# Kernel tuning notes

Hardware: AMD Instinct MI355X
Metric: run time of the kernel (lower is better)

The kernel has to match this reference:

```python
import jax, jax.numpy as jnp
import numpy as np

B, T, D = 2, 4096, 768
H = 12
HD = D // H  # 64
SCALE = 1.0 / np.sqrt(HD)


def setup_inputs() -> dict:
    key = jax.random.key(0)
    k1, k2, k3 = jax.random.split(key, 3)
    x = jax.random.normal(k1, (B, T, D), dtype=jnp.float32)
    W_qkv = jax.random.normal(k2, (D, 3 * D), dtype=jnp.float32) * (1.0 / np.sqrt(D))
    b_qkv = jnp.zeros((3 * D,), dtype=jnp.float32)
    W_out = jax.random.normal(k3, (D, D), dtype=jnp.float32) * (1.0 / np.sqrt(D))
    b_out = jnp.zeros((D,), dtype=jnp.float32)
    return {"x": x, "W_qkv": W_qkv, "b_qkv": b_qkv, "W_out": W_out, "b_out": b_out}


def reference(x, W_qkv, b_qkv, W_out, b_out):
    Bx, Tx, C = x.shape
    qkv = x @ W_qkv + b_qkv                                  # [B,T,3D]
    qkv = qkv.reshape(Bx, Tx, 3, H, HD).transpose(2, 0, 3, 1, 4)  # [3,B,H,T,hd]
    q, k, v = qkv[0], qkv[1], qkv[2]
    scores = jnp.einsum('bhqd,bhkd->bhqk', q, k) * SCALE      # [B,H,T,T]
    causal = jnp.tril(jnp.ones((Tx, Tx), dtype=bool))
    scores = jnp.where(causal[None, None], scores, -jnp.inf)
    attn = jax.nn.softmax(scores, axis=-1)
    out = jnp.einsum('bhqk,bhkd->bhqd', attn, v)              # [B,H,T,hd]
    out = out.transpose(0, 2, 1, 3).reshape(Bx, Tx, C)        # [B,T,D]
    return out @ W_out + b_out
```

## Files before the change

### kernel.cpp

```cpp
#include <hip/hip_runtime.h>
#include <cstdint>
#include <cstddef>

typedef _Float16 f16x8 __attribute__((ext_vector_type(8)));
typedef _Float16 f16x4 __attribute__((ext_vector_type(4)));
typedef float    f32x4 __attribute__((ext_vector_type(4)));

#define AS_GLOBAL __attribute__((address_space(1)))
#define AS_LDS    __attribute__((address_space(3)))

__device__ __forceinline__ void load16_to_lds(const _Float16* g, _Float16* l) {
    __builtin_amdgcn_global_load_lds((const AS_GLOBAL void*)g, (AS_LDS void*)l, 16, 0, 0);
}

#define BB   2
#define TT   4096
#define DD   768
#define NH   12
#define HDIM 64
#define D3   2304
#define SC2  (0.125f * 1.44269504088896f)

__global__ __launch_bounds__(256) void prep(const float* __restrict__ x,
                                            _Float16* __restrict__ Xh,
                                            const float* __restrict__ Wqkv,
                                            _Float16* __restrict__ Wqkvt,
                                            const float* __restrict__ Wout,
                                            _Float16* __restrict__ Wot) {
    const int bid = blockIdx.x, tid = threadIdx.x;
    if (bid < 6144) {
        const int i = bid * 1024 + tid * 4;
        float4 v = *(const float4*)(x + i);
        f16x4 h;
        h[0] = (_Float16)v.x; h[1] = (_Float16)v.y;
        h[2] = (_Float16)v.z; h[3] = (_Float16)v.w;
        *(f16x4*)(Xh + i) = h;
        return;
    }
    __shared__ float tile[32][33];
    const float* in; _Float16* out; int C, bx, by;
    if (bid < 7872) {
        const int t = bid - 6144;
        in = Wqkv; out = Wqkvt; C = 2304;
        bx = (t % 72) * 32; by = (t / 72) * 32;
    } else {
        const int t = bid - 7872;
        in = Wout; out = Wot; C = 768;
        bx = (t % 24) * 32; by = (t / 24) * 32;
    }
    const int R = 768;
    const int tx = tid & 31, ty = tid >> 5;
#pragma unroll
    for (int j = 0; j < 32; j += 8)
        tile[ty + j][tx] = in[(size_t)(by + ty + j) * C + bx + tx];
    __syncthreads();
#pragma unroll
    for (int j = 0; j < 32; j += 8)
        out[(size_t)(bx + ty + j) * R + by + tx] = (_Float16)tile[tx][ty + j];
}

template <typename OutT>
__device__ __forceinline__ void gemm_body(const _Float16* __restrict__ A,
                                          const _Float16* __restrict__ Bt,
                                          const float* __restrict__ bias, bool bias_row,
                                          OutT* __restrict__ C, int N, int K,
                                          int m0, int n0,
                                          _Float16* As, _Float16* Bs) {
    const int tid  = threadIdx.x;
    const int wave = tid >> 6, lane = tid & 63, quad = lane >> 4, l16 = lane & 15;
    const int wm = (wave & 1) * 64, wn = (wave >> 1) * 64;
    const int rowc = lane >> 3, part = lane & 7;

    f32x4 acc[4][4];
#pragma unroll
    for (int i = 0; i < 4; ++i)
#pragma unroll
        for (int n = 0; n < 4; ++n) acc[i][n] = f32x4{0.f, 0.f, 0.f, 0.f};

    for (int k0 = 0; k0 < K; k0 += 64) {
        __syncthreads();
#pragma unroll
        for (int cc = 0; cc < 4; ++cc) {
            const int ch = wave * 4 + cc;
            load16_to_lds(A  + (size_t)(m0 + ch * 8 + rowc) * K + k0 + part * 8,
                          As + ch * 512);
            load16_to_lds(Bt + (size_t)(n0 + ch * 8 + rowc) * K + k0 + part * 8,
                          Bs + ch * 512);
        }
        __syncthreads();
#pragma unroll
        for (int i = 0; i < 4; ++i) {
            f16x8 a0 = *(const f16x8*)(As + (wm + i * 16 + l16) * 64 + quad * 8);
            f16x8 a1 = *(const f16x8*)(As + (wm + i * 16 + l16) * 64 + 32 + quad * 8);
#pragma unroll
            for (int n = 0; n < 4; ++n) {
                f16x8 b0 = *(const f16x8*)(Bs + (wn + n * 16 + l16) * 64 + quad * 8);
                f16x8 b1 = *(const f16x8*)(Bs + (wn + n * 16 + l16) * 64 + 32 + quad * 8);
                acc[i][n] = __builtin_amdgcn_mfma_f32_16x16x32_f16(a0, b0, acc[i][n], 0, 0, 0);
                acc[i][n] = __builtin_amdgcn_mfma_f32_16x16x32_f16(a1, b1, acc[i][n], 0, 0, 0);
            }
        }
    }
#pragma unroll
    for (int i = 0; i < 4; ++i)
#pragma unroll
        for (int n = 0; n < 4; ++n)
#pragma unroll
            for (int r = 0; r < 4; ++r) {
                const int row = m0 + wm + i * 16 + quad * 4 + r;
                const int col = n0 + wn + n * 16 + l16;
                const float bv = bias_row ? bias[row] : bias[col];
                C[(size_t)row * N + col] = (OutT)(acc[i][n][r] + bv);
            }
}

__global__ __launch_bounds__(256) void gemm_qkv(const _Float16* __restrict__ Xh,
                                                const _Float16* __restrict__ Wqkvt,
                                                const float* __restrict__ bqkv,
                                                _Float16* __restrict__ QKh,
                                                _Float16* __restrict__ VtG) {
    __shared__ __align__(16) _Float16 As[128 * 64];
    __shared__ __align__(16) _Float16 Bs[128 * 64];
    const int bid = blockIdx.x;
    if (bid < 768) {
        const int xcd = bid & 7, j = bid >> 3;
        const int by = xcd + 8 * (j / 12);
        const int bx = j % 12;
        gemm_body<_Float16>(Xh, Wqkvt, bqkv, false, QKh, 1536, DD,
                            by * 128, bx * 128, As, Bs);
    } else {
        const int t = bid - 768;
        const int xcd = t & 7, j = t >> 3;
        const int bx = xcd + 8 * (j / 6);
        const int by = j % 6;
        gemm_body<_Float16>(Wqkvt + (size_t)1536 * DD, Xh, bqkv + 1536, true, VtG,
                            8192, DD, by * 128, bx * 128, As, Bs);
    }
}

__global__ __launch_bounds__(256) void gemm_out(const _Float16* __restrict__ A,
                                                const _Float16* __restrict__ Bt,
                                                const float* __restrict__ bias,
                                                float* __restrict__ C) {
    __shared__ __align__(16) _Float16 As[64 * 64];
    __shared__ __align__(16) _Float16 Bs[128 * 64];
    const int L = blockIdx.x;
    const int xcd = L & 7, j = L >> 3;
    const int by = xcd + 8 * (j / 6);
    const int bx = j % 6;
    const int m0 = by * 64, n0 = bx * 128;
    const int N = DD, K = DD;
    const int tid  = threadIdx.x;
    const int wave = tid >> 6, lane = tid & 63, quad = lane >> 4, l16 = lane & 15;
    const int wm = (wave & 1) * 32, wn = (wave >> 1) * 64;
    const int rowc = lane >> 3, part = lane & 7;

    f32x4 acc[2][4];
#pragma unroll
    for (int i = 0; i < 2; ++i)
#pragma unroll
        for (int n = 0; n < 4; ++n) acc[i][n] = f32x4{0.f, 0.f, 0.f, 0.f};

    for (int k0 = 0; k0 < K; k0 += 64) {
        __syncthreads();
#pragma unroll
        for (int cc = 0; cc < 2; ++cc) {
            const int ch = wave * 2 + cc;
            load16_to_lds(A + (size_t)(m0 + ch * 8 + rowc) * K + k0 + part * 8,
                          As + ch * 512);
        }
#pragma unroll
        for (int cc = 0; cc < 4; ++cc) {
            const int ch = wave * 4 + cc;
            load16_to_lds(Bt + (size_t)(n0 + ch * 8 + rowc) * K + k0 + part * 8,
                          Bs + ch * 512);
        }
        __syncthreads();
#pragma unroll
        for (int i = 0; i < 2; ++i) {
            f16x8 a0 = *(const f16x8*)(As + (wm + i * 16 + l16) * 64 + quad * 8);
            f16x8 a1 = *(const f16x8*)(As + (wm + i * 16 + l16) * 64 + 32 + quad * 8);
#pragma unroll
            for (int n = 0; n < 4; ++n) {
                f16x8 b0 = *(const f16x8*)(Bs + (wn + n * 16 + l16) * 64 + quad * 8);
                f16x8 b1 = *(const f16x8*)(Bs + (wn + n * 16 + l16) * 64 + 32 + quad * 8);
                acc[i][n] = __builtin_amdgcn_mfma_f32_16x16x32_f16(a0, b0, acc[i][n], 0, 0, 0);
                acc[i][n] = __builtin_amdgcn_mfma_f32_16x16x32_f16(a1, b1, acc[i][n], 0, 0, 0);
            }
        }
    }
#pragma unroll
    for (int i = 0; i < 2; ++i)
#pragma unroll
        for (int n = 0; n < 4; ++n)
#pragma unroll
            for (int r = 0; r < 4; ++r) {
                const int row = m0 + wm + i * 16 + quad * 4 + r;
                const int col = n0 + wn + n * 16 + l16;
                C[(size_t)row * N + col] = acc[i][n][r] + bias[col];
            }
}

__global__ __launch_bounds__(256, 5) void attn_kernel(const _Float16* __restrict__ qk,
                                                      const _Float16* __restrict__ vt,
                                                      _Float16* __restrict__ ao) {
    __shared__ __align__(16) _Float16 Ks[2][64 * 64];
    __shared__ __align__(16) _Float16 Vs[2][64 * 64];

    const int L    = blockIdx.x;
    const int xcd  = L & 7;
    const int r_   = L >> 3;
    const int gIdx = r_ % 3;
    const int qt   = 63 - r_ / 3;
    const int g    = gIdx * 8 + xcd;
    const int b = g / NH, h = g % NH;

    const int tid = threadIdx.x;
    const int wave = tid >> 6, lane = tid & 63, quad = lane >> 4, l16 = lane & 15;
    const int wq = wave >> 1, wk = wave & 1;

    f16x4 ones4;
#pragma unroll
    for (int j = 0; j < 4; ++j) ones4[j] = (_Float16)1.0f;

    int vK[2], vV[2];
#pragma unroll
    for (int p = 0; p < 2; ++p) {
        const int j   = wave * 16 + p * 8 + (lane >> 3);
        const int cdk = (lane & 7) ^ (j & 7);
        const int cdv = (lane & 7) ^ (((j & 3) << 1) | ((j >> 2) & 1));
        vK[p] = (b * TT + j) * 1536 + DD + h * HDIM + cdk * 8;
        vV[p] = (h * HDIM + j) * 8192 + b * TT + cdv * 8;
    }
    auto stage = [&](int buf, int k0) {
        const int kK = k0 * 1536;
#pragma unroll
        for (int p = 0; p < 2; ++p) {
            load16_to_lds(qk + (vK[p] + kK), Ks[buf] + (wave * 16 + p * 8) * 64);
            load16_to_lds(vt + (vV[p] + k0), Vs[buf] + (wave * 16 + p * 8) * 64);
        }
    };

    const int q0 = qt * 64;
    const int nkt = qt + 1;
    const int qrow0 = q0 + wq * 32;
    const int qr_lane = qrow0 + l16;
    const int rv = ((l16 & 3) << 1) | ((l16 >> 2) & 1);
    f16x8 aq[2][2];
#pragma unroll
    for (int mq = 0; mq < 2; ++mq) {
        const int qoff = (b * TT + qrow0 + mq * 16 + l16) * 1536 + h * HDIM + quad * 8;
        const _Float16 sc = (_Float16)SC2;
        aq[mq][0] = *(const f16x8*)(qk + qoff) * sc;
        aq[mq][1] = *(const f16x8*)(qk + qoff + 32) * sc;
    }
    f32x4 o[2][4], lac[2];
#pragma unroll
    for (int mq = 0; mq < 2; ++mq) {
#pragma unroll
        for (int n = 0; n < 4; ++n) o[mq][n] = f32x4{0.f, 0.f, 0.f, 0.f};
        lac[mq] = f32x4{0.f, 0.f, 0.f, 0.f};
    }

    stage(0, 0);
    int cur = 0;
    for (int kt = 0; kt < nkt; ++kt) {
        __syncthreads();
        if (kt + 1 < nkt) stage(cur ^ 1, (kt + 1) * 64);

        f32x4 s[2][2];
        f16x4 pa[2][2];
#pragma unroll
        for (int mq = 0; mq < 2; ++mq)
#pragma unroll
            for (int n1 = 0; n1 < 2; ++n1) s[mq][n1] = f32x4{0.f, 0.f, 0.f, 0.f};

        auto qk_half = [&](int n1) {
#pragma unroll
            for (int kh = 0; kh < 2; ++kh) {
                const int rowK = (wk * 2 + n1) * 16 + l16;
                const int pos = (kh * 4 + quad) ^ (l16 & 7);
                f16x8 bk = *(const f16x8*)(Ks[cur] + rowK * 64 + pos * 8);
                s[0][n1] = __builtin_amdgcn_mfma_f32_16x16x32_f16(bk, aq[0][kh], s[0][n1], 0, 0, 0);
                s[1][n1] = __builtin_amdgcn_mfma_f32_16x16x32_f16(bk, aq[1][kh], s[1][n1], 0, 0, 0);
            }
        };
        auto mask_half = [&](int n1) {
#pragma unroll
            for (int mq = 0; mq < 2; ++mq) {
                const int qr = qr_lane + mq * 16;
                const int kg0 = kt * 64 + wk * 32 + n1 * 16 + quad * 4;
#pragma unroll
                for (int r = 0; r < 4; ++r)
                    if (kg0 + r > qr) s[mq][n1][r] = -1e30f;
            }
        };
        auto exp_half = [&](int n1) {
#pragma unroll
            for (int mq = 0; mq < 2; ++mq)
#pragma unroll
                for (int r = 0; r < 4; ++r)
                    pa[mq][n1][r] = (_Float16)__builtin_amdgcn_exp2f(s[mq][n1][r]);
        };
        auto pv_half = [&](int n1) {
            f16x4 ap0 = pa[0][n1], ap1 = pa[1][n1];
            lac[0] = __builtin_amdgcn_mfma_f32_16x16x16f16(ap0, ones4, lac[0], 0, 0, 0);
            lac[1] = __builtin_amdgcn_mfma_f32_16x16x16f16(ap1, ones4, lac[1], 0, 0, 0);
#pragma unroll
            for (int n = 0; n < 4; ++n) {
                const int rowV = n * 16 + l16;
                const int lc  = wk * 4 + n1 * 2 + (quad >> 1);
                const int pc  = lc ^ rv;
                f16x4 bv = *(const f16x4*)(Vs[cur] + rowV * 64 + pc * 8 + (quad & 1) * 4);
                o[0][n] = __builtin_amdgcn_mfma_f32_16x16x16f16(ap0, bv, o[0][n], 0, 0, 0);
                o[1][n] = __builtin_amdgcn_mfma_f32_16x16x16f16(ap1, bv, o[1][n], 0, 0, 0);
            }
        };

        const bool last = (kt == nkt - 1);
        __builtin_amdgcn_s_setprio(1);
        qk_half(0);
        __builtin_amdgcn_s_setprio(0);
        if (last) mask_half(0);
        exp_half(0);
        __builtin_amdgcn_s_setprio(1);
        qk_half(1);
        pv_half(0);
        __builtin_amdgcn_s_setprio(0);
        if (last) mask_half(1);
        exp_half(1);
        __builtin_amdgcn_s_setprio(1);
        pv_half(1);
        __builtin_amdgcn_s_setprio(0);
        cur ^= 1;
    }

    __syncthreads();
    float* const Ksf = (float*)&Ks[0][0];
    float* const Vsf = (float*)&Vs[0][0];
    if (wk) {
#pragma unroll
        for (int mq = 0; mq < 2; ++mq) {
            if (l16 == 0)
                *(f32x4*)(Vsf + wq * 32 + mq * 16 + quad * 4) = lac[mq];
#pragma unroll
            for (int n = 0; n < 4; ++n)
                *(f32x4*)(Ksf + wq * 2048 + (mq * 4 + n) * 256 + lane * 4) = o[mq][n];
        }
    }
    __syncthreads();
    if (!wk) {
#pragma unroll
        for (int mq = 0; mq < 2; ++mq) {
            f32x4 lp = *(const f32x4*)(Vsf + wq * 32 + mq * 16 + quad * 4);
            f32x4 inv;
#pragma unroll
            for (int r = 0; r < 4; ++r) inv[r] = 1.0f / (lac[mq][r] + lp[r]);
#pragma unroll
            for (int n = 0; n < 4; ++n) {
                f32x4 op = *(const f32x4*)(Ksf + wq * 2048 + (mq * 4 + n) * 256 + lane * 4);
#pragma unroll
                for (int r = 0; r < 4; ++r) {
                    const int ooff = (b * TT + qrow0 + mq * 16 + quad * 4 + r) * DD + h * HDIM + l16;
                    ao[ooff + n * 16] = (_Float16)((o[mq][n][r] + op[r]) * inv[r]);
                }
            }
        }
    }
}

extern "C" void kernel_launch(void* const* d_in, const int* in_sizes, int n_in,
                              void* d_out, int out_size, void* d_ws, size_t ws_size,
                              hipStream_t stream) {
    const float* x     = (const float*)d_in[0];
    const float* Wqkv  = (const float*)d_in[1];
    const float* bqkv  = (const float*)d_in[2];
    const float* Wout  = (const float*)d_in[3];
    const float* bout  = (const float*)d_in[4];
    float* out = (float*)d_out;

    char* ws = (char*)d_ws;
    _Float16* Xh    = (_Float16*)ws;  ws += (size_t)BB * TT * DD * 2;
    _Float16* Wqkvt = (_Float16*)ws;  ws += (size_t)D3 * DD * 2;
    _Float16* Wot   = (_Float16*)ws;  ws += (size_t)DD * DD * 2;
    _Float16* QKh   = (_Float16*)ws;  ws += (size_t)BB * TT * 1536 * 2;
    _Float16* VtG   = (_Float16*)ws;  ws += (size_t)DD * BB * TT * 2;
    _Float16* AOh   = (_Float16*)ws;  ws += (size_t)BB * TT * DD * 2;

    prep<<<8448, 256, 0, stream>>>(x, Xh, Wqkv, Wqkvt, Wout, Wot);

    gemm_qkv<<<1152, 256, 0, stream>>>(Xh, Wqkvt, bqkv, QKh, VtG);

    attn_kernel<<<1536, 256, 0, stream>>>(QKh, VtG, AOh);

    gemm_out<<<768, 256, 0, stream>>>(AOh, Wot, bout, out);
}
```

Measured before the change: 234.8 us.

## Double-buffer GEMM LDS tiles with K=32 stages to overlap loads and MFMA

The QKV and output-projection GEMMs switch from a single-buffered K=64 tile to a double-buffered K=32 tile. The next stage's global-to-LDS loads are issued before computing on the current buffer, and one barrier per iteration replaces two. The aim is to hide global load latency behind MFMA work. In exchange there are twice as many iterations and barriers. With a 32-element row stride in LDS, the fragment reads may hit bank conflicts.

```diff
diff --git a/kernel.cpp b/kernel.cpp
--- a/kernel.cpp
+++ b/kernel.cpp
@@ -69,7 +69,6 @@
     const int tid  = threadIdx.x;
     const int wave = tid >> 6, lane = tid & 63, quad = lane >> 4, l16 = lane & 15;
     const int wm = (wave & 1) * 64, wn = (wave >> 1) * 64;
-    const int rowc = lane >> 3, part = lane & 7;
 
     f32x4 acc[4][4];
 #pragma unroll
@@ -77,29 +76,34 @@
 #pragma unroll
         for (int n = 0; n < 4; ++n) acc[i][n] = f32x4{0.f, 0.f, 0.f, 0.f};
 
-    for (int k0 = 0; k0 < K; k0 += 64) {
+    auto stage = [&](int buf, int k0) {
+#pragma unroll
+        for (int p = 0; p < 2; ++p) {
+            const int j = p * 256 + wave * 64 + lane;
+            const int row = j >> 2, part = j & 3;
+            load16_to_lds(A  + (size_t)(m0 + row) * K + k0 + part * 8,
+                          As + buf * 4096 + (p * 256 + wave * 64) * 8);
+            load16_to_lds(Bt + (size_t)(n0 + row) * K + k0 + part * 8,
+                          Bs + buf * 4096 + (p * 256 + wave * 64) * 8);
+        }
+    };
+
+    const int nt = K >> 5;
+    stage(0, 0);
+    int cur = 0;
+    for (int t = 0; t < nt; ++t) {
         __syncthreads();
-#pragma unroll
-        for (int cc = 0; cc < 4; ++cc) {
-            const int ch = wave * 4 + cc;
-            load16_to_lds(A  + (size_t)(m0 + ch * 8 + rowc) * K + k0 + part * 8,
-                          As + ch * 512);
-            load16_to_lds(Bt + (size_t)(n0 + ch * 8 + rowc) * K + k0 + part * 8,
-                          Bs + ch * 512);
-        }
-        __syncthreads();
+        if (t + 1 < nt) stage(cur ^ 1, (t + 1) * 32);
 #pragma unroll
         for (int i = 0; i < 4; ++i) {
-            f16x8 a0 = *(const f16x8*)(As + (wm + i * 16 + l16) * 64 + quad * 8);
-            f16x8 a1 = *(const f16x8*)(As + (wm + i * 16 + l16) * 64 + 32 + quad * 8);
+            f16x8 a = *(const f16x8*)(As + cur * 4096 + (wm + i * 16 + l16) * 32 + quad * 8);
 #pragma unroll
             for (int n = 0; n < 4; ++n) {
-                f16x8 b0 = *(const f16x8*)(Bs + (wn + n * 16 + l16) * 64 + quad * 8);
-                f16x8 b1 = *(const f16x8*)(Bs + (wn + n * 16 + l16) * 64 + 32 + quad * 8);
-                acc[i][n] = __builtin_amdgcn_mfma_f32_16x16x32_f16(a0, b0, acc[i][n], 0, 0, 0);
-                acc[i][n] = __builtin_amdgcn_mfma_f32_16x16x32_f16(a1, b1, acc[i][n], 0, 0, 0);
-            }
-        }
+                f16x8 b = *(const f16x8*)(Bs + cur * 4096 + (wn + n * 16 + l16) * 32 + quad * 8);
+                acc[i][n] = __builtin_amdgcn_mfma_f32_16x16x32_f16(a, b, acc[i][n], 0, 0, 0);
+            }
+        }
+        cur ^= 1;
     }
 #pragma unroll
     for (int i = 0; i < 4; ++i)
@@ -119,8 +123,8 @@
                                                 const float* __restrict__ bqkv,
                                                 _Float16* __restrict__ QKh,
                                                 _Float16* __restrict__ VtG) {
-    __shared__ __align__(16) _Float16 As[128 * 64];
-    __shared__ __align__(16) _Float16 Bs[128 * 64];
+    __shared__ __align__(16) _Float16 As[2 * 128 * 32];
+    __shared__ __align__(16) _Float16 Bs[2 * 128 * 32];
     const int bid = blockIdx.x;
     if (bid < 768) {
         const int xcd = bid & 7, j = bid >> 3;
@@ -142,8 +146,8 @@
                                                 const _Float16* __restrict__ Bt,
                                                 const float* __restrict__ bias,
                                                 float* __restrict__ C) {
-    __shared__ __align__(16) _Float16 As[64 * 64];
-    __shared__ __align__(16) _Float16 Bs[128 * 64];
+    __shared__ __align__(16) _Float16 As[2 * 64 * 32];
+    __shared__ __align__(16) _Float16 Bs[2 * 128 * 32];
     const int L = blockIdx.x;
     const int xcd = L & 7, j = L >> 3;
     const int by = xcd + 8 * (j / 6);
@@ -153,7 +157,6 @@
     const int tid  = threadIdx.x;
     const int wave = tid >> 6, lane = tid & 63, quad = lane >> 4, l16 = lane & 15;
     const int wm = (wave & 1) * 32, wn = (wave >> 1) * 64;
-    const int rowc = lane >> 3, part = lane & 7;
 
     f32x4 acc[2][4];
 #pragma unroll
@@ -161,33 +164,38 @@
 #pragma unroll
         for (int n = 0; n < 4; ++n) acc[i][n] = f32x4{0.f, 0.f, 0.f, 0.f};
 
-    for (int k0 = 0; k0 < K; k0 += 64) {
+    auto stage = [&](int buf, int k0) {
+        {
+            const int jj = wave * 64 + lane;
+            const int row = jj >> 2, part = jj & 3;
+            load16_to_lds(A + (size_t)(m0 + row) * K + k0 + part * 8,
+                          As + buf * 2048 + (wave * 64) * 8);
+        }
+#pragma unroll
+        for (int p = 0; p < 2; ++p) {
+            const int jj = p * 256 + wave * 64 + lane;
+            const int row = jj >> 2, part = jj & 3;
+            load16_to_lds(Bt + (size_t)(n0 + row) * K + k0 + part * 8,
+                          Bs + buf * 4096 + (p * 256 + wave * 64) * 8);
+        }
+    };
+
+    const int nt = K >> 5;
+    stage(0, 0);
+    int cur = 0;
+    for (int t = 0; t < nt; ++t) {
         __syncthreads();
-#pragma unroll
-        for (int cc = 0; cc < 2; ++cc) {
-            const int ch = wave * 2 + cc;
-            load16_to_lds(A + (size_t)(m0 + ch * 8 + rowc) * K + k0 + part * 8,
-                          As + ch * 512);
-        }
-#pragma unroll
-        for (int cc = 0; cc < 4; ++cc) {
-            const int ch = wave * 4 + cc;
-            load16_to_lds(Bt + (size_t)(n0 + ch * 8 + rowc) * K + k0 + part * 8,
-                          Bs + ch * 512);
-        }
-        __syncthreads();
+        if (t + 1 < nt) stage(cur ^ 1, (t + 1) * 32);
 #pragma unroll
         for (int i = 0; i < 2; ++i) {
-            f16x8 a0 = *(const f16x8*)(As + (wm + i * 16 + l16) * 64 + quad * 8);
-            f16x8 a1 = *(const f16x8*)(As + (wm + i * 16 + l16) * 64 + 32 + quad * 8);
+            f16x8 a = *(const f16x8*)(As + cur * 2048 + (wm + i * 16 + l16) * 32 + quad * 8);
 #pragma unroll
             for (int n = 0; n < 4; ++n) {
-                f16x8 b0 = *(const f16x8*)(Bs + (wn + n * 16 + l16) * 64 + quad * 8);
-                f16x8 b1 = *(const f16x8*)(Bs + (wn + n * 16 + l16) * 64 + 32 + quad * 8);
-                acc[i][n] = __builtin_amdgcn_mfma_f32_16x16x32_f16(a0, b0, acc[i][n], 0, 0, 0);
-                acc[i][n] = __builtin_amdgcn_mfma_f32_16x16x32_f16(a1, b1, acc[i][n], 0, 0, 0);
-            }
-        }
+                f16x8 b = *(const f16x8*)(Bs + cur * 4096 + (wn + n * 16 + l16) * 32 + quad * 8);
+                acc[i][n] = __builtin_amdgcn_mfma_f32_16x16x32_f16(a, b, acc[i][n], 0, 0, 0);
+            }
+        }
+        cur ^= 1;
     }
 #pragma unroll
     for (int i = 0; i < 2; ++i)
```

New measurement: 231.5 us. No clear change (-1.4%).
